# Optimization experiments

Measured on AMD Instinct MI355X. Metric: run time of the kernel, lower is better.

Reference implementation:

```python
import jax, jax.numpy as jnp
import numpy as np

B, C_IN, N = 64, 1, 8192
WIDTH, MODES, NLAYERS = 64, 16, 4


def setup_inputs() -> dict:
    key = jax.random.key(0)
    ks = jax.random.split(key, 10)
    scale = 1.0 / (WIDTH * WIDTH)
    inp = {
        "x": jax.random.normal(ks[0], (B, C_IN, N), dtype=jnp.float32),
        # lifting p: Linear(2, width)
        "p_w": jax.random.normal(ks[1], (WIDTH, 2), dtype=jnp.float32) * 0.5,
        "p_b": jax.random.normal(ks[2], (WIDTH,), dtype=jnp.float32) * 0.1,
        # 4 spectral conv weights, complex stored as real/imag (uniform like torch.rand cfloat)
        "sc_wr": scale * jax.random.uniform(ks[3], (NLAYERS, WIDTH, WIDTH, MODES), dtype=jnp.float32),
        "sc_wi": scale * jax.random.uniform(ks[4], (NLAYERS, WIDTH, WIDTH, MODES), dtype=jnp.float32),
        # 4 pointwise (1x1) conv weights/biases
        "w_w": jax.random.normal(ks[5], (NLAYERS, WIDTH, WIDTH), dtype=jnp.float32) / np.sqrt(WIDTH),
        "w_b": jax.random.normal(ks[6], (NLAYERS, WIDTH), dtype=jnp.float32) * 0.1,
        # projection q: Linear(width, 1)
        "q_w": jax.random.normal(ks[7], (1, WIDTH), dtype=jnp.float32) / np.sqrt(WIDTH),
        "q_b": jax.random.normal(ks[8], (1,), dtype=jnp.float32) * 0.1,
    }
    return inp


def spectral_conv(x, wr, wi, n):
    # x: [b, i, n] real; weights complex [i, o, modes]
    x_ft = jnp.fft.rfft(x, axis=-1)                      # [b, i, n//2+1] complex
    w = (wr + 1j * wi).astype(jnp.complex64)
    out_modes = jnp.einsum('bix,iox->box', x_ft[:, :, :MODES], w)
    out_ft = jnp.zeros((x.shape[0], w.shape[1], n // 2 + 1), dtype=jnp.complex64)
    out_ft = out_ft.at[:, :, :MODES].set(out_modes)
    return jnp.fft.irfft(out_ft, n=n, axis=-1)


def reference(x, p_w, p_b, sc_wr, sc_wi, w_w, w_b, q_w, q_b):
    b, _, n = x.shape
    grid = jnp.broadcast_to(jnp.linspace(0.0, 1.0, n, dtype=jnp.float32)[None, None, :], (b, 1, n))
    h = jnp.concatenate([x, grid], axis=1)               # [b, 2, n]
    # lifting: Linear over channel dim
    h = jnp.einsum('bcn,wc->bwn', h, p_w) + p_b[None, :, None]
    for l in range(NLAYERS):
        x1 = spectral_conv(h, sc_wr[l], sc_wi[l], n)
        x2 = jnp.einsum('bin,oi->bon', h, w_w[l]) + w_b[l][None, :, None]
        h = jax.nn.gelu(x1 + x2, approximate=False)
    out = jnp.einsum('bwn,ow->bon', h, q_w) + q_b[None, :, None]  # [b, 1, n]
    return out
```

## Files before the change

### kernel.cpp

```cpp
#include <hip/hip_runtime.h>
#include <math.h>


typedef _Float16 f16;
typedef _Float16 f16x2 __attribute__((ext_vector_type(2)));
typedef _Float16 f16x4 __attribute__((ext_vector_type(4)));
typedef _Float16 f16x8 __attribute__((ext_vector_type(8)));
typedef float    f32x2 __attribute__((ext_vector_type(2)));
typedef float    f32x4 __attribute__((ext_vector_type(4)));
typedef unsigned int u32;

#define BB 64
#define NN 8192

#define HT_S 64
#define HO_S 136
#define BF_S 136

__device__ __forceinline__ int ht_swz(int n) { return ((n & 7) ^ ((n >> 3) & 7)) << 3; }

__device__ __forceinline__ float gelu_f(float v) {
    float x  = v * 0.70710678118654752f;
    float ax = fabsf(x);
    float t  = __builtin_amdgcn_rcpf(fmaf(0.3275911f, ax, 1.0f));
    float p  = fmaf(1.061405429f, t, -1.453152027f);
    p = fmaf(p, t, 1.421413741f);
    p = fmaf(p, t, -0.284496736f);
    p = fmaf(p, t, 0.254829592f);
    p = p * t;
    float e  = __expf(-x * x);
    float er = fmaf(-p, e, 1.0f);
    er = copysignf(er, x);
    return 0.5f * fmaf(v, er, v);
}

__global__ __launch_bounds__(256) void fill_basis(f16* __restrict__ basF,
                                                  f16* __restrict__ basI,
                                                  const float* __restrict__ w_w,
                                                  f16* __restrict__ Wh,
                                                  float* __restrict__ Sz) {
    int n = blockIdx.x * 256 + threadIdx.x;
    f16 row[32];
#pragma unroll
    for (int k = 0; k < 16; ++k) {
        float s, c;
        sincospif((float)(k * n) * (1.0f / 4096.0f), &s, &c);
        basF[k * NN + n]        = (f16)c;
        basF[(16 + k) * NN + n] = (f16)(-s);
        row[2 * k]     = (f16)c;
        row[2 * k + 1] = (f16)s;
    }
#pragma unroll
    for (int q = 0; q < 4; ++q) *(f16x8*)&basI[n * 32 + 8 * q] = *(f16x8*)&row[8 * q];
    Wh[n]        = (f16)w_w[n];
    Wh[n + 8192] = (f16)w_w[n + 8192];
    f32x4* S4 = (f32x4*)Sz;
    f32x4 z = {0.f, 0.f, 0.f, 0.f};
#pragma unroll
    for (int u = 0; u < 4; ++u) S4[n * 4 + u] = z;
}

__global__ __launch_bounds__(1024) void mode_mix(float* __restrict__ S,
                                                 const float* __restrict__ wr,
                                                 const float* __restrict__ wi,
                                                 f16* __restrict__ Mph) {
    int b = blockIdx.x, t = threadIdx.x;
    __shared__ float Ss[32 * 66];
    if (t < 512) {
        f32x4 v = *(const f32x4*)&S[b * 2048 + t * 4];
        int rw = t >> 4, cl = (t & 15) * 4;
#pragma unroll
        for (int e = 0; e < 4; ++e) Ss[rw * 66 + cl + e] = v[e];
    }
    __syncthreads();
    *(f32x2*)&S[b * 2048 + t * 2] = (f32x2){0.f, 0.f};

    int o = t >> 4, k = t & 15;
    const float* wrp = wr + o * 16 + k;
    const float* wip = wi + o * 16 + k;
    float ar = 0.f, ai = 0.f;
#pragma unroll 8
    for (int i = 0; i < 64; ++i) {
        float sr = Ss[k * 66 + i], si = Ss[(16 + k) * 66 + i];
        float wrv = wrp[i * 1024];
        float wiv = wip[i * 1024];
        ar = fmaf(sr, wrv, ar); ar = fmaf(-si, wiv, ar);
        ai = fmaf(sr, wiv, ai); ai = fmaf(si, wrv, ai);
    }
    float sc = (k == 0 ? 1.0f : 2.0f) * (1.0f / 8192.0f);
    f16x2 outv = { (f16)(sc * ar), (f16)(-sc * ai) };
    *(f16x2*)&Mph[b * 2048 + o * 32 + 2 * k] = outv;
}

__device__ __forceinline__ void dft_accum(const f16* Hout, const f16* BasF,
                                          f32x4 sacc[2], int lane, int wv) {
    int q = lane >> 4, l15 = lane & 15;
    int o = (wv << 4) + l15;
#pragma unroll
    for (int ks = 0; ks < 4; ++ks) {
        f16x8 bh = *(const f16x8*)&Hout[o * HO_S + ks * 32 + q * 8];
#pragma unroll
        for (int mt = 0; mt < 2; ++mt) {
            f16x8 af = *(const f16x8*)&BasF[(mt * 16 + l15) * BF_S + ks * 32 + q * 8];
            sacc[mt] = __builtin_amdgcn_mfma_f32_16x16x32_f16(af, bh, sacc[mt], 0, 0, 0);
        }
    }
}

__device__ __forceinline__ void dft_accum_g(const f16* Hout, const f16* __restrict__ basF_g,
                                            int n0, f32x4 sacc[2], int lane, int wv) {
    int q = lane >> 4, l15 = lane & 15;
    int o = (wv << 4) + l15;
#pragma unroll
    for (int ks = 0; ks < 4; ++ks) {
        f16x8 bh = *(const f16x8*)&Hout[o * HO_S + ks * 32 + q * 8];
#pragma unroll
        for (int mt = 0; mt < 2; ++mt) {
            f16x8 af = *(const f16x8*)&basF_g[(mt * 16 + l15) * NN + n0 + ks * 32 + q * 8];
            sacc[mt] = __builtin_amdgcn_mfma_f32_16x16x32_f16(af, bh, sacc[mt], 0, 0, 0);
        }
    }
}

__device__ __forceinline__ void dft_flush(const f32x4 sacc[2], float* __restrict__ S,
                                          int b, int lane, int wv) {
    int q = lane >> 4, l15 = lane & 15;
#pragma unroll
    for (int mt = 0; mt < 2; ++mt)
#pragma unroll
        for (int r = 0; r < 4; ++r)
            atomicAdd(&S[(b * 32 + mt * 16 + q * 4 + r) * 64 + (wv << 4) + l15],
                      sacc[mt][r]);
}

__global__ __launch_bounds__(256, 3) void lift_kernel(const float* __restrict__ x,
                                                      const float* __restrict__ p_w,
                                                      const float* __restrict__ p_b,
                                                      f16* __restrict__ h,
                                                      const f16* __restrict__ basF_g,
                                                      float* __restrict__ S) {
    __shared__ f16 Hout[64 * HO_S];
    __shared__ f16 BasF[32 * BF_S];
    int t = threadIdx.x;
    int b = blockIdx.x >> 5;
    int g = blockIdx.x & 31;
    int lane = t & 63, wv = t >> 6;
    int ns = (t & 15) << 3;

    float w0[4], w1[4], pb[4];
#pragma unroll
    for (int r = 0; r < 4; ++r) {
        int o = (t >> 4) + 16 * r;
        w0[r] = p_w[2 * o]; w1[r] = p_w[2 * o + 1]; pb[r] = p_b[o];
    }

    f32x4 X[2][2];
#pragma unroll
    for (int tile = 0; tile < 2; ++tile) {
        int n0 = ((g << 1) + tile) << 7;
        X[tile][0] = *(const f32x4*)&x[(b << 13) + n0 + ns];
        X[tile][1] = *(const f32x4*)&x[(b << 13) + n0 + ns + 4];
    }

    f32x4 sacc[2] = {{0.f,0.f,0.f,0.f},{0.f,0.f,0.f,0.f}};
#pragma unroll
    for (int tile = 0; tile < 2; ++tile) {
        int n0 = ((g << 1) + tile) << 7;
#pragma unroll
        for (int r = 0; r < 4; ++r) {
            int o = (t >> 4) + 16 * r;
            f16 vals[8];
#pragma unroll
            for (int j = 0; j < 8; ++j) {
                int n = n0 + ns + j;
                float xv = X[tile][j >> 2][j & 3];
                vals[j] = (f16)(w0[r] * xv + w1[r] * ((float)n * (1.0f / 8191.0f)) + pb[r]);
            }
            *(f16x8*)&Hout[o * HO_S + ns] = *(f16x8*)vals;
            *(f16x8*)(h + (((size_t)(b * 64 + o)) << 13) + n0 + ns) = *(f16x8*)vals;
        }
#pragma unroll
        for (int u = 0; u < 2; ++u) {
            int km = t >> 3, nn = (t & 7) * 16 + u * 8;
            *(f16x8*)&BasF[km * BF_S + nn] = *(const f16x8*)&basF_g[km * NN + n0 + nn];
        }
        __syncthreads();
        dft_accum(Hout, BasF, sacc, lane, wv);
        if (tile == 0) __syncthreads();
    }
    dft_flush(sacc, S, b, lane, wv);
}

template <int DO_DFT>
__global__ __launch_bounds__(256, 3) void layer_kernel(f16* __restrict__ h,
                                                       const f16* __restrict__ Wl_h,
                                                       const float* __restrict__ bl,
                                                       const f16* __restrict__ Mph,
                                                       const f16* __restrict__ basF_g,
                                                       const f16* __restrict__ basI_g,
                                                       float* __restrict__ S,
                                                       const float* __restrict__ q_w,
                                                       const float* __restrict__ q_b,
                                                       float* __restrict__ out) {
    __shared__ __align__(16) char pool[DO_DFT ? 17408 : 16384];
    f16* Ht   = (f16*)pool;
    f16* Hout = (f16*)pool;
    __shared__ float bls[64];
    int t = threadIdx.x;
    int b = blockIdx.x >> 5;
    int g = blockIdx.x & 31;
    f16* hbase = h + (((size_t)(b * 64)) << 13);
    int lane = t & 63, wv = t >> 6;
    int q = lane >> 4, l15 = lane & 15;
    int blk = t >> 1, half = t & 1;
    int ig = blk >> 4, nb = blk & 15;
    int i0 = ig << 3, nst = nb << 3;
    int swz = nb & 7;
    int n0_0 = (g << 1) << 7, n0_1 = ((g << 1) + 1) << 7;
    f16* hbt0 = hbase + n0_0;
    f16* hbt1 = hbase + n0_1;

    f16x8 Bw[4][2], Bm[4];
#pragma unroll
    for (int ct = 0; ct < 4; ++ct) {
#pragma unroll
        for (int ks = 0; ks < 2; ++ks)
            Bw[ct][ks] = *(const f16x8*)&Wl_h[(ct * 16 + l15) * 64 + ks * 32 + q * 8];
        Bm[ct] = *(const f16x8*)&Mph[b * 2048 + (ct * 16 + l15) * 32 + q * 8];
    }
    if (t < 64) bls[t] = bl[t];

    f16x8 R0[4];
#pragma unroll
    for (int k = 0; k < 4; ++k)
        R0[k] = *(const f16x8*)(hbt0 + ((size_t)(i0 + half * 4 + k) << 13) + nst);
    f16x8 Ab0[2];
#pragma unroll
    for (int mtl = 0; mtl < 2; ++mtl)
        Ab0[mtl] = *(const f16x8*)&basI_g[(size_t)(n0_0 + (2 * wv + mtl) * 16 + l15) * 32 + q * 8];
    {
        const u32* rd = (const u32*)R0;
#pragma unroll
        for (int j = 0; j < 8; ++j) {
            u32 sel = (j & 1) ? 0x07060302u : 0x05040100u;
            int jd = j >> 1;
            u32 oo[2] __attribute__((aligned(8)));
            oo[0] = __builtin_amdgcn_perm(rd[4 + jd],  rd[jd],      sel);
            oo[1] = __builtin_amdgcn_perm(rd[12 + jd], rd[8 + jd],  sel);
            int col = (i0 ^ ((j ^ swz) << 3)) + half * 4;
            *(f16x4*)&Ht[(nst + j) * HT_S + col] = *(const f16x4*)oo;
        }
    }
    __syncthreads();

    f16x8 R1[4];
#pragma unroll
    for (int k = 0; k < 4; ++k)
        R1[k] = *(const f16x8*)(hbt1 + ((size_t)(i0 + half * 4 + k) << 13) + nst);
    f16x8 Ab1[2];
#pragma unroll
    for (int mtl = 0; mtl < 2; ++mtl)
        Ab1[mtl] = *(const f16x8*)&basI_g[(size_t)(n0_1 + (2 * wv + mtl) * 16 + l15) * 32 + q * 8];

    float bv[4];
#pragma unroll
    for (int ct = 0; ct < 4; ++ct) bv[ct] = bls[ct * 16 + l15];

    f32x4 sacc[2] = {{0.f,0.f,0.f,0.f},{0.f,0.f,0.f,0.f}};

    f32x4 acc[4][2];
#pragma unroll
    for (int ct = 0; ct < 4; ++ct)
#pragma unroll
        for (int m = 0; m < 2; ++m) acc[ct][m] = (f32x4){0.f, 0.f, 0.f, 0.f};
#pragma unroll
    for (int mtl = 0; mtl < 2; ++mtl) {
        int nrow = (2 * wv + mtl) * 16 + l15;
        const f16* hrow = &Ht[nrow * HT_S];
        int g3 = ht_swz(nrow);
#pragma unroll
        for (int ks = 0; ks < 2; ++ks) {
            f16x8 Ah = *(const f16x8*)&hrow[(ks * 32 + q * 8) ^ g3];
#pragma unroll
            for (int ct = 0; ct < 4; ++ct)
                acc[ct][mtl] = __builtin_amdgcn_mfma_f32_16x16x32_f16(
                    Ah, Bw[ct][ks], acc[ct][mtl], 0, 0, 0);
        }
#pragma unroll
        for (int ct = 0; ct < 4; ++ct)
            acc[ct][mtl] = __builtin_amdgcn_mfma_f32_16x16x32_f16(
                Ab0[mtl], Bm[ct], acc[ct][mtl], 0, 0, 0);
    }

    if (DO_DFT) {
        __syncthreads();
#pragma unroll
        for (int ct = 0; ct < 4; ++ct) {
            int o = ct * 16 + l15;
#pragma unroll
            for (int mtl = 0; mtl < 2; ++mtl) {
                int nbase = (2 * wv + mtl) * 16 + q * 4;
                float gg[4];
#pragma unroll
                for (int r = 0; r < 4; ++r)
                    gg[r] = gelu_f(acc[ct][mtl][r] + bv[ct]);
                f16x2 lo = __builtin_bit_cast(f16x2, __builtin_amdgcn_cvt_pkrtz(gg[0], gg[1]));
                f16x2 hi = __builtin_bit_cast(f16x2, __builtin_amdgcn_cvt_pkrtz(gg[2], gg[3]));
                f16x4 pk = {lo[0], lo[1], hi[0], hi[1]};
                *(f16x4*)&Hout[o * HO_S + nbase] = pk;
            }
        }
        __syncthreads();
#pragma unroll
        for (int r = 0; r < 4; ++r) {
            int o = (t >> 4) + 16 * r;
            int ns2 = (t & 15) << 3;
            *(f16x8*)(hbt0 + ((size_t)o << 13) + ns2) = *(f16x8*)&Hout[o * HO_S + ns2];
        }
        dft_accum_g(Hout, basF_g, n0_0, sacc, lane, wv);
        __syncthreads();
        {
            const u32* rd = (const u32*)R1;
#pragma unroll
            for (int j = 0; j < 8; ++j) {
                u32 sel = (j & 1) ? 0x07060302u : 0x05040100u;
                int jd = j >> 1;
                u32 oo[2] __attribute__((aligned(8)));
                oo[0] = __builtin_amdgcn_perm(rd[4 + jd],  rd[jd],     sel);
                oo[1] = __builtin_amdgcn_perm(rd[12 + jd], rd[8 + jd], sel);
                int col = (i0 ^ ((j ^ swz) << 3)) + half * 4;
                *(f16x4*)&Ht[(nst + j) * HT_S + col] = *(const f16x4*)oo;
            }
        }
        __syncthreads();
    } else {
        float qv[4];
#pragma unroll
        for (int ct = 0; ct < 4; ++ct) qv[ct] = q_w[ct * 16 + l15];
        float part[2][4] = {{0.f,0.f,0.f,0.f},{0.f,0.f,0.f,0.f}};
#pragma unroll
        for (int ct = 0; ct < 4; ++ct)
#pragma unroll
            for (int mtl = 0; mtl < 2; ++mtl)
#pragma unroll
                for (int r = 0; r < 4; ++r)
                    part[mtl][r] = fmaf(qv[ct], gelu_f(acc[ct][mtl][r] + bv[ct]), part[mtl][r]);
#pragma unroll
        for (int mtl = 0; mtl < 2; ++mtl)
#pragma unroll
            for (int r = 0; r < 4; ++r) {
                float s = part[mtl][r];
#pragma unroll
                for (int m = 1; m < 16; m <<= 1) s += __shfl_xor(s, m, 64);
                if (l15 == 0)
                    out[(b << 13) + n0_0 + (2 * wv + mtl) * 16 + q * 4 + r] = s + q_b[0];
            }
        __syncthreads();
        {
            const u32* rd = (const u32*)R1;
#pragma unroll
            for (int j = 0; j < 8; ++j) {
                u32 sel = (j & 1) ? 0x07060302u : 0x05040100u;
                int jd = j >> 1;
                u32 oo[2] __attribute__((aligned(8)));
                oo[0] = __builtin_amdgcn_perm(rd[4 + jd],  rd[jd],     sel);
                oo[1] = __builtin_amdgcn_perm(rd[12 + jd], rd[8 + jd], sel);
                int col = (i0 ^ ((j ^ swz) << 3)) + half * 4;
                *(f16x4*)&Ht[(nst + j) * HT_S + col] = *(const f16x4*)oo;
            }
        }
        __syncthreads();
    }

#pragma unroll
    for (int ct = 0; ct < 4; ++ct)
#pragma unroll
        for (int m = 0; m < 2; ++m) acc[ct][m] = (f32x4){0.f, 0.f, 0.f, 0.f};
#pragma unroll
    for (int mtl = 0; mtl < 2; ++mtl) {
        int nrow = (2 * wv + mtl) * 16 + l15;
        const f16* hrow = &Ht[nrow * HT_S];
        int g3 = ht_swz(nrow);
#pragma unroll
        for (int ks = 0; ks < 2; ++ks) {
            f16x8 Ah = *(const f16x8*)&hrow[(ks * 32 + q * 8) ^ g3];
#pragma unroll
            for (int ct = 0; ct < 4; ++ct)
                acc[ct][mtl] = __builtin_amdgcn_mfma_f32_16x16x32_f16(
                    Ah, Bw[ct][ks], acc[ct][mtl], 0, 0, 0);
        }
#pragma unroll
        for (int ct = 0; ct < 4; ++ct)
            acc[ct][mtl] = __builtin_amdgcn_mfma_f32_16x16x32_f16(
                Ab1[mtl], Bm[ct], acc[ct][mtl], 0, 0, 0);
    }

    if (DO_DFT) {
        __syncthreads();
#pragma unroll
        for (int ct = 0; ct < 4; ++ct) {
            int o = ct * 16 + l15;
#pragma unroll
            for (int mtl = 0; mtl < 2; ++mtl) {
                int nbase = (2 * wv + mtl) * 16 + q * 4;
                float gg[4];
#pragma unroll
                for (int r = 0; r < 4; ++r)
                    gg[r] = gelu_f(acc[ct][mtl][r] + bv[ct]);
                f16x2 lo = __builtin_bit_cast(f16x2, __builtin_amdgcn_cvt_pkrtz(gg[0], gg[1]));
                f16x2 hi = __builtin_bit_cast(f16x2, __builtin_amdgcn_cvt_pkrtz(gg[2], gg[3]));
                f16x4 pk = {lo[0], lo[1], hi[0], hi[1]};
                *(f16x4*)&Hout[o * HO_S + nbase] = pk;
            }
        }
        __syncthreads();
#pragma unroll
        for (int r = 0; r < 4; ++r) {
            int o = (t >> 4) + 16 * r;
            int ns2 = (t & 15) << 3;
            *(f16x8*)(hbt1 + ((size_t)o << 13) + ns2) = *(f16x8*)&Hout[o * HO_S + ns2];
        }
        dft_accum_g(Hout, basF_g, n0_1, sacc, lane, wv);
        dft_flush(sacc, S, b, lane, wv);
    } else {
        float qv[4];
#pragma unroll
        for (int ct = 0; ct < 4; ++ct) qv[ct] = q_w[ct * 16 + l15];
        float part[2][4] = {{0.f,0.f,0.f,0.f},{0.f,0.f,0.f,0.f}};
#pragma unroll
        for (int ct = 0; ct < 4; ++ct)
#pragma unroll
            for (int mtl = 0; mtl < 2; ++mtl)
#pragma unroll
                for (int r = 0; r < 4; ++r)
                    part[mtl][r] = fmaf(qv[ct], gelu_f(acc[ct][mtl][r] + bv[ct]), part[mtl][r]);
#pragma unroll
        for (int mtl = 0; mtl < 2; ++mtl)
#pragma unroll
            for (int r = 0; r < 4; ++r) {
                float s = part[mtl][r];
#pragma unroll
                for (int m = 1; m < 16; m <<= 1) s += __shfl_xor(s, m, 64);
                if (l15 == 0)
                    out[(b << 13) + n0_1 + (2 * wv + mtl) * 16 + q * 4 + r] = s + q_b[0];
            }
    }
}

extern "C" void kernel_launch(void* const* d_in, const int* in_sizes, int n_in,
                              void* d_out, int out_size, void* d_ws, size_t ws_size,
                              hipStream_t stream) {
    const float* x     = (const float*)d_in[0];
    const float* p_w   = (const float*)d_in[1];
    const float* p_b   = (const float*)d_in[2];
    const float* sc_wr = (const float*)d_in[3];
    const float* sc_wi = (const float*)d_in[4];
    const float* w_w   = (const float*)d_in[5];
    const float* w_b   = (const float*)d_in[6];
    const float* q_w   = (const float*)d_in[7];
    const float* q_b   = (const float*)d_in[8];
    float* out = (float*)d_out;

    char* ws = (char*)d_ws;
    f16*   h    = (f16*)ws;
    float* S    = (float*)(ws + 67108864ull);
    f16*   Mph  = (f16*)(ws + 67633152ull);
    f16*   basF = (f16*)(ws + 67895296ull);
    f16*   basI = (f16*)(ws + 68419584ull);
    f16*   Wh   = (f16*)(ws + 68943872ull);

    hipLaunchKernelGGL(fill_basis, dim3(NN / 256), dim3(256), 0, stream,
                       basF, basI, w_w, Wh, S);
    hipLaunchKernelGGL(lift_kernel, dim3(BB * 32), dim3(256), 0, stream,
                       x, p_w, p_b, h, basF, S);
    for (int l = 0; l < 4; ++l) {
        hipLaunchKernelGGL(mode_mix, dim3(BB), dim3(1024), 0, stream,
                           S, sc_wr + l * 65536, sc_wi + l * 65536, Mph);
        if (l < 3) {
            hipLaunchKernelGGL((layer_kernel<1>), dim3(BB * 32), dim3(256), 0, stream,
                               h, Wh + l * 4096, w_b + l * 64, Mph, basF, basI, S,
                               q_w, q_b, out);
        } else {
            hipLaunchKernelGGL((layer_kernel<0>), dim3(BB * 32), dim3(256), 0, stream,
                               h, Wh + l * 4096, w_b + l * 64, Mph, basF, basI, S,
                               q_w, q_b, out);
        }
    }
}
```

Baseline: 293.2 us.

## Store hidden activations position-major to avoid transposes on load

Changes the global layout of the hidden activation buffer h from channel-major [b][ch][n] to position-major [b][n][ch]. The writer now transposes from LDS once via perm, and the layer kernels load contiguous 64-channel rows straight into the swizzled Ht tile with no register transpose. Ht and Hout are split into separate LDS arrays so two barriers can be dropped, which raises LDS use in the DFT variant. The intent is to cut ALU permute work and get more contiguous global accesses when reading h.

New measurement: 303.1 us. 3.4% more time.

```diff
diff --git a/kernel.cpp b/kernel.cpp
--- a/kernel.cpp
+++ b/kernel.cpp
@@ -92,6 +92,27 @@
     *(f16x2*)&Mph[b * 2048 + o * 32 + 2 * k] = outv;
 }
 
+__device__ __forceinline__ void store_h_T(const f16* Hout, f16* __restrict__ hdst,
+                                          int t) {
+    int blk = t >> 1, half = t & 1;
+    int ob = blk >> 4, nb2 = blk & 15;
+    int o0 = ob << 3, ns = nb2 << 3;
+    f16x8 R[4];
+#pragma unroll
+    for (int k = 0; k < 4; ++k)
+        R[k] = *(const f16x8*)&Hout[(o0 + half * 4 + k) * HO_S + ns];
+    const u32* rd = (const u32*)R;
+#pragma unroll
+    for (int j = 0; j < 8; ++j) {
+        u32 sel = (j & 1) ? 0x07060302u : 0x05040100u;
+        int jd = j >> 1;
+        u32 oo[2] __attribute__((aligned(8)));
+        oo[0] = __builtin_amdgcn_perm(rd[4 + jd],  rd[jd],     sel);
+        oo[1] = __builtin_amdgcn_perm(rd[12 + jd], rd[8 + jd], sel);
+        *(f16x4*)&hdst[((ns + j) << 6) + o0 + half * 4] = *(const f16x4*)oo;
+    }
+}
+
 __device__ __forceinline__ void dft_accum(const f16* Hout, const f16* BasF,
                                           f32x4 sacc[2], int lane, int wv) {
     int q = lane >> 4, l15 = lane & 15;
@@ -146,6 +167,7 @@
     int g = blockIdx.x & 31;
     int lane = t & 63, wv = t >> 6;
     int ns = (t & 15) << 3;
+    f16* hbase = h + ((size_t)b << 19);
 
     float w0[4], w1[4], pb[4];
 #pragma unroll
@@ -177,7 +199,6 @@
                 vals[j] = (f16)(w0[r] * xv + w1[r] * ((float)n * (1.0f / 8191.0f)) + pb[r]);
             }
             *(f16x8*)&Hout[o * HO_S + ns] = *(f16x8*)vals;
-            *(f16x8*)(h + (((size_t)(b * 64 + o)) << 13) + n0 + ns) = *(f16x8*)vals;
         }
 #pragma unroll
         for (int u = 0; u < 2; ++u) {
@@ -186,6 +207,7 @@
         }
         __syncthreads();
         dft_accum(Hout, BasF, sacc, lane, wv);
+        store_h_T(Hout, hbase + ((size_t)n0 << 6), t);
         if (tile == 0) __syncthreads();
     }
     dft_flush(sacc, S, b, lane, wv);
@@ -202,23 +224,20 @@
                                                        const float* __restrict__ q_w,
                                                        const float* __restrict__ q_b,
                                                        float* __restrict__ out) {
-    __shared__ __align__(16) char pool[DO_DFT ? 17408 : 16384];
-    f16* Ht   = (f16*)pool;
-    f16* Hout = (f16*)pool;
+    __shared__ __align__(16) f16 Ht[128 * HT_S];
+    __shared__ __align__(16) f16 Hout[DO_DFT ? 64 * HO_S : 8];
     __shared__ float bls[64];
     int t = threadIdx.x;
     int b = blockIdx.x >> 5;
     int g = blockIdx.x & 31;
-    f16* hbase = h + (((size_t)(b * 64)) << 13);
+    f16* hbase = h + ((size_t)b << 19);
     int lane = t & 63, wv = t >> 6;
     int q = lane >> 4, l15 = lane & 15;
-    int blk = t >> 1, half = t & 1;
-    int ig = blk >> 4, nb = blk & 15;
-    int i0 = ig << 3, nst = nb << 3;
-    int swz = nb & 7;
     int n0_0 = (g << 1) << 7, n0_1 = ((g << 1) + 1) << 7;
-    f16* hbt0 = hbase + n0_0;
-    f16* hbt1 = hbase + n0_1;
+    f16* hbt0 = hbase + ((size_t)n0_0 << 6);
+    f16* hbt1 = hbase + ((size_t)n0_1 << 6);
+    int srow = t >> 1, shalf = t & 1;
+    int sg3 = ht_swz(srow);
 
     f16x8 Bw[4][2], Bm[4];
 #pragma unroll
@@ -230,33 +249,25 @@
     }
     if (t < 64) bls[t] = bl[t];
 
-    f16x8 R0[4];
-#pragma unroll
-    for (int k = 0; k < 4; ++k)
-        R0[k] = *(const f16x8*)(hbt0 + ((size_t)(i0 + half * 4 + k) << 13) + nst);
+    {
+        const f16* src = hbt0 + ((size_t)srow << 6) + shalf * 32;
+        f16* drow = &Ht[srow * HT_S];
+#pragma unroll
+        for (int u = 0; u < 4; ++u) {
+            int c = shalf * 32 + u * 8;
+            *(f16x8*)&drow[c ^ sg3] = *(const f16x8*)&src[u * 8];
+        }
+    }
     f16x8 Ab0[2];
 #pragma unroll
     for (int mtl = 0; mtl < 2; ++mtl)
         Ab0[mtl] = *(const f16x8*)&basI_g[(size_t)(n0_0 + (2 * wv + mtl) * 16 + l15) * 32 + q * 8];
-    {
-        const u32* rd = (const u32*)R0;
-#pragma unroll
-        for (int j = 0; j < 8; ++j) {
-            u32 sel = (j & 1) ? 0x07060302u : 0x05040100u;
-            int jd = j >> 1;
-            u32 oo[2] __attribute__((aligned(8)));
-            oo[0] = __builtin_amdgcn_perm(rd[4 + jd],  rd[jd],      sel);
-            oo[1] = __builtin_amdgcn_perm(rd[12 + jd], rd[8 + jd],  sel);
-            int col = (i0 ^ ((j ^ swz) << 3)) + half * 4;
-            *(f16x4*)&Ht[(nst + j) * HT_S + col] = *(const f16x4*)oo;
-        }
-    }
     __syncthreads();
 
     f16x8 R1[4];
 #pragma unroll
-    for (int k = 0; k < 4; ++k)
-        R1[k] = *(const f16x8*)(hbt1 + ((size_t)(i0 + half * 4 + k) << 13) + nst);
+    for (int u = 0; u < 4; ++u)
+        R1[u] = *(const f16x8*)(hbt1 + ((size_t)srow << 6) + shalf * 32 + u * 8);
     f16x8 Ab1[2];
 #pragma unroll
     for (int mtl = 0; mtl < 2; ++mtl)
@@ -293,7 +304,6 @@
     }
 
     if (DO_DFT) {
-        __syncthreads();
 #pragma unroll
         for (int ct = 0; ct < 4; ++ct) {
             int o = ct * 16 + l15;
@@ -311,25 +321,14 @@
             }
         }
         __syncthreads();
-#pragma unroll
-        for (int r = 0; r < 4; ++r) {
-            int o = (t >> 4) + 16 * r;
-            int ns2 = (t & 15) << 3;
-            *(f16x8*)(hbt0 + ((size_t)o << 13) + ns2) = *(f16x8*)&Hout[o * HO_S + ns2];
-        }
+        store_h_T(Hout, hbt0, t);
         dft_accum_g(Hout, basF_g, n0_0, sacc, lane, wv);
-        __syncthreads();
         {
-            const u32* rd = (const u32*)R1;
-#pragma unroll
-            for (int j = 0; j < 8; ++j) {
-                u32 sel = (j & 1) ? 0x07060302u : 0x05040100u;
-                int jd = j >> 1;
-                u32 oo[2] __attribute__((aligned(8)));
-                oo[0] = __builtin_amdgcn_perm(rd[4 + jd],  rd[jd],     sel);
-                oo[1] = __builtin_amdgcn_perm(rd[12 + jd], rd[8 + jd], sel);
-                int col = (i0 ^ ((j ^ swz) << 3)) + half * 4;
-                *(f16x4*)&Ht[(nst + j) * HT_S + col] = *(const f16x4*)oo;
+            f16* drow = &Ht[srow * HT_S];
+#pragma unroll
+            for (int u = 0; u < 4; ++u) {
+                int c = shalf * 32 + u * 8;
+                *(f16x8*)&drow[c ^ sg3] = R1[u];
             }
         }
         __syncthreads();
@@ -357,16 +356,11 @@
             }
         __syncthreads();
         {
-            const u32* rd = (const u32*)R1;
-#pragma unroll
-            for (int j = 0; j < 8; ++j) {
-                u32 sel = (j & 1) ? 0x07060302u : 0x05040100u;
-                int jd = j >> 1;
-                u32 oo[2] __attribute__((aligned(8)));
-                oo[0] = __builtin_amdgcn_perm(rd[4 + jd],  rd[jd],     sel);
-                oo[1] = __builtin_amdgcn_perm(rd[12 + jd], rd[8 + jd], sel);
-                int col = (i0 ^ ((j ^ swz) << 3)) + half * 4;
-                *(f16x4*)&Ht[(nst + j) * HT_S + col] = *(const f16x4*)oo;
+            f16* drow = &Ht[srow * HT_S];
+#pragma unroll
+            for (int u = 0; u < 4; ++u) {
+                int c = shalf * 32 + u * 8;
+                *(f16x8*)&drow[c ^ sg3] = R1[u];
             }
         }
         __syncthreads();
@@ -396,7 +390,6 @@
     }
 
     if (DO_DFT) {
-        __syncthreads();
 #pragma unroll
         for (int ct = 0; ct < 4; ++ct) {
             int o = ct * 16 + l15;
@@ -414,12 +407,7 @@
             }
         }
         __syncthreads();
-#pragma unroll
-        for (int r = 0; r < 4; ++r) {
-            int o = (t >> 4) + 16 * r;
-            int ns2 = (t & 15) << 3;
-            *(f16x8*)(hbt1 + ((size_t)o << 13) + ns2) = *(f16x8*)&Hout[o * HO_S + ns2];
-        }
+        store_h_T(Hout, hbt1, t);
         dft_accum_g(Hout, basF_g, n0_1, sacc, lane, wv);
         dft_flush(sacc, S, b, lane, wv);
     } else {
```
